# Kernel optimization log

Hardware: AMD Instinct MI355X
Metric: run time of the kernel (lower is better)

The kernel has to match this reference:

```python
import jax, jax.numpy as jnp
import numpy as np
from jax import lax

VOCAB = 32000; D = 1024; NL = 4; DI = 2048; S = 16; R = 64; DC = 4
B = 1; L = 1024; EPS = 1e-5


def setup_inputs() -> dict:
    key = jax.random.key(0)
    ks = jax.random.split(key, 16)
    def n(k, shape, s=0.02):
        return jax.random.normal(k, shape, dtype=jnp.float32) * s
    return dict(
        tokens=jax.random.randint(ks[0], (B, L), 0, VOCAB),
        embed=n(ks[1], (VOCAB, D)),
        norm_w=jnp.ones((NL, D), jnp.float32) + n(ks[2], (NL, D)),
        in_proj_w=n(ks[3], (NL, 2 * DI, D)),
        conv_w=n(ks[4], (NL, DI, DC), 0.1),
        conv_b=n(ks[5], (NL, DI)),
        x_proj_w=n(ks[6], (NL, R + 2 * S, DI)),
        dt_proj_w=n(ks[7], (NL, DI, R), 0.1),
        dt_proj_b=n(ks[8], (NL, DI), 0.5),
        A_log=n(ks[9], (NL, DI, S), 0.5),
        D_param=jnp.ones((NL, DI), jnp.float32) + n(ks[10], (NL, DI)),
        out_proj_w=n(ks[11], (NL, D, DI)),
        norm_f_w=jnp.ones((D,), jnp.float32),
        lm_head_w=n(ks[12], (VOCAB, D)),
    )


def _rmsnorm(x, w):
    return x * lax.rsqrt(jnp.mean(x * x, axis=-1, keepdims=True) + EPS) * w


def _mamba_block(x, norm_w, in_w, cw, cb, xw, dtw, dtb, a_log, dp, ow):
    # x: [B, L, D]
    res = x
    x = _rmsnorm(x, norm_w)
    xz = jnp.einsum('bld,ed->ble', x, in_w)      # [B, L, 2*DI]
    u, z = xz[..., :DI], xz[..., DI:]
    # depthwise causal conv over time
    u = jnp.swapaxes(u, 1, 2)                    # [B, DI, L]
    u = lax.conv_general_dilated(u, cw[:, None, :], (1,), [(DC - 1, 0)],
                                 feature_group_count=DI,
                                 dimension_numbers=('NCH', 'OIH', 'NCH'))
    u = jax.nn.silu(u + cb[None, :, None])
    u = jnp.swapaxes(u, 1, 2)                    # [B, L, DI]
    # input-dependent SSM params
    dbc = jnp.einsum('bld,ed->ble', u, xw)       # [B, L, R+2S]
    dt = jax.nn.softplus(jnp.einsum('blr,dr->bld', dbc[..., :R], dtw) + dtb)
    Bm = dbc[..., R:R + S]                       # [B, L, S]
    Cm = dbc[..., R + S:]                        # [B, L, S]
    A = -jnp.exp(a_log)                          # [DI, S]
    dA = jnp.exp(dt[..., None] * A)              # [B, L, DI, S]
    dBu = (dt * u)[..., None] * Bm[:, :, None, :]  # [B, L, DI, S]
    # selective scan over time
    def step(h, inp):
        a_t, b_t, c_t = inp
        h = a_t * h + b_t                        # [B, DI, S]
        y = jnp.einsum('bds,bs->bd', h, c_t)
        return h, y
    h0 = jnp.zeros((x.shape[0], DI, S), x.dtype)
    _, ys = lax.scan(step, h0, (jnp.moveaxis(dA, 1, 0), jnp.moveaxis(dBu, 1, 0), jnp.moveaxis(Cm, 1, 0)))
    y = jnp.moveaxis(ys, 0, 1) + u * dp          # [B, L, DI]
    y = y * jax.nn.silu(z)
    return res + jnp.einsum('bld,od->blo', y, ow)


def reference(tokens, embed, norm_w, in_proj_w, conv_w, conv_b, x_proj_w,
              dt_proj_w, dt_proj_b, A_log, D_param, out_proj_w, norm_f_w, lm_head_w):
    x = embed[tokens]                            # [B, L, D]
    for i in range(NL):
        x = _mamba_block(x, norm_w[i], in_proj_w[i], conv_w[i], conv_b[i],
                         x_proj_w[i], dt_proj_w[i], dt_proj_b[i], A_log[i],
                         D_param[i], out_proj_w[i])
    x = _rmsnorm(x, norm_f_w)
    return jnp.einsum('bld,vd->blv', x, lm_head_w)  # [B, L, VOCAB]
```

## Files before the change

kernel.cpp:

```cpp
#include <hip/hip_runtime.h>
#include <hip/hip_bf16.h>
#include <math.h>


typedef __attribute__((ext_vector_type(8))) short bf16x8;
typedef __attribute__((ext_vector_type(4))) float f32x4;

__device__ __forceinline__ short f2bf(float f) {
  union { float f; unsigned u; } v; v.f = f;
  unsigned u = v.u;
  unsigned r = (u + 0x7FFFu + ((u >> 16) & 1u)) >> 16;
  return (short)r;
}

__device__ __forceinline__ bf16x8 pack8(float4 a, float4 b) {
  bf16x8 r;
  r[0] = f2bf(a.x); r[1] = f2bf(a.y); r[2] = f2bf(a.z); r[3] = f2bf(a.w);
  r[4] = f2bf(b.x); r[5] = f2bf(b.y); r[6] = f2bf(b.z); r[7] = f2bf(b.w);
  return r;
}

__device__ __forceinline__ unsigned cvtpk(float lo, float hi) {
  unsigned r;
  asm("v_cvt_pk_bf16_f32 %0, %1, %2" : "=v"(r) : "v"(lo), "v"(hi));
  return r;
}

__device__ __forceinline__ float softplus_f(float x) {
  return (x > 20.f) ? x : log1pf(__expf(x));
}

__device__ __forceinline__ void gl_lds16(const void* g, void* l) {
  void* gnc = (void*)g;
  __builtin_amdgcn_global_load_lds((__attribute__((address_space(1))) void*)gnc,
                                   (__attribute__((address_space(3))) void*)l, 16, 0, 0);
}

__global__ __launch_bounds__(256) void cvt4_k(const float* __restrict__ s0, unsigned short* __restrict__ d0, int nb0,
                                              const float* __restrict__ s1, unsigned short* __restrict__ d1, int nb1,
                                              const float* __restrict__ s2, unsigned short* __restrict__ d2, int nb2,
                                              const float* __restrict__ s3, unsigned short* __restrict__ d3, int nb3) {
  int b = blockIdx.x;
  const float* s; unsigned short* d; int lb;
  if (b < nb0) { s = s0; d = d0; lb = b; }
  else if (b < nb0 + nb1) { s = s1; d = d1; lb = b - nb0; }
  else if (b < nb0 + nb1 + nb2) { s = s2; d = d2; lb = b - nb0 - nb1; }
  else { s = s3; d = d3; lb = b - nb0 - nb1 - nb2; }
  size_t base = (size_t)lb * 1024;
#pragma unroll
  for (int u = 0; u < 4; ++u) {
    size_t idx = base + u * 256 + threadIdx.x;
    const float4* p = (const float4*)(s + idx * 8);
    float4 a = p[0], bq = p[1];
    uint4 w;
    w.x = cvtpk(a.x, a.y); w.y = cvtpk(a.z, a.w);
    w.z = cvtpk(bq.x, bq.y); w.w = cvtpk(bq.z, bq.w);
    *(uint4*)(d + idx * 8) = w;
  }
}

__global__ __launch_bounds__(256) void embed_rms_k(const int* __restrict__ tok,
                                                   const float* __restrict__ emb,
                                                   const float* __restrict__ w,
                                                   float* __restrict__ x,
                                                   unsigned short* __restrict__ xn16) {
  int l = blockIdx.x;
  int t = tok[l];
  float4 v = ((const float4*)(emb + (size_t)t * 1024))[threadIdx.x];
  ((float4*)(x + (size_t)l * 1024))[threadIdx.x] = v;
  float ss = v.x * v.x + v.y * v.y + v.z * v.z + v.w * v.w;
  ss += __shfl_down(ss, 32); ss += __shfl_down(ss, 16); ss += __shfl_down(ss, 8);
  ss += __shfl_down(ss, 4);  ss += __shfl_down(ss, 2);  ss += __shfl_down(ss, 1);
  __shared__ float wsum[4];
  if ((threadIdx.x & 63) == 0) wsum[threadIdx.x >> 6] = ss;
  __syncthreads();
  float tot = wsum[0] + wsum[1] + wsum[2] + wsum[3];
  float sc = rsqrtf(tot * (1.0f / 1024.0f) + 1e-5f);
  float4 wv = ((const float4*)w)[threadIdx.x];
  ushort4 o;
  o.x = (unsigned short)f2bf(v.x * sc * wv.x);
  o.y = (unsigned short)f2bf(v.y * sc * wv.y);
  o.z = (unsigned short)f2bf(v.z * sc * wv.z);
  o.w = (unsigned short)f2bf(v.w * sc * wv.w);
  *(ushort4*)(xn16 + (size_t)l * 1024 + threadIdx.x * 4) = o;
}

__global__ __launch_bounds__(256) void rmsnorm16_k(const float* __restrict__ x,
                                                   const float* __restrict__ w,
                                                   unsigned short* __restrict__ y) {
  int l = blockIdx.x;
  const float4* xr = (const float4*)(x + (size_t)l * 1024);
  float4 v = xr[threadIdx.x];
  float ss = v.x * v.x + v.y * v.y + v.z * v.z + v.w * v.w;
  ss += __shfl_down(ss, 32); ss += __shfl_down(ss, 16); ss += __shfl_down(ss, 8);
  ss += __shfl_down(ss, 4);  ss += __shfl_down(ss, 2);  ss += __shfl_down(ss, 1);
  __shared__ float wsum[4];
  if ((threadIdx.x & 63) == 0) wsum[threadIdx.x >> 6] = ss;
  __syncthreads();
  float tot = wsum[0] + wsum[1] + wsum[2] + wsum[3];
  float sc = rsqrtf(tot * (1.0f / 1024.0f) + 1e-5f);
  float4 wv = ((const float4*)w)[threadIdx.x];
  ushort4 o;
  o.x = (unsigned short)f2bf(v.x * sc * wv.x);
  o.y = (unsigned short)f2bf(v.y * sc * wv.y);
  o.z = (unsigned short)f2bf(v.z * sc * wv.z);
  o.w = (unsigned short)f2bf(v.w * sc * wv.w);
  *(ushort4*)(y + (size_t)l * 1024 + threadIdx.x * 4) = o;
}

__global__ __launch_bounds__(256) void rmsnorm_k(const float* __restrict__ x,
                                                 const float* __restrict__ w,
                                                 float* __restrict__ y) {
  int l = blockIdx.x;
  const float4* xr = (const float4*)(x + (size_t)l * 1024);
  float4 v = xr[threadIdx.x];
  float ss = v.x * v.x + v.y * v.y + v.z * v.z + v.w * v.w;
  ss += __shfl_down(ss, 32); ss += __shfl_down(ss, 16); ss += __shfl_down(ss, 8);
  ss += __shfl_down(ss, 4);  ss += __shfl_down(ss, 2);  ss += __shfl_down(ss, 1);
  __shared__ float wsum[4];
  if ((threadIdx.x & 63) == 0) wsum[threadIdx.x >> 6] = ss;
  __syncthreads();
  float tot = wsum[0] + wsum[1] + wsum[2] + wsum[3];
  float sc = rsqrtf(tot * (1.0f / 1024.0f) + 1e-5f);
  float4 wv = ((const float4*)w)[threadIdx.x];
  float4 o;
  o.x = v.x * sc * wv.x; o.y = v.y * sc * wv.y;
  o.z = v.z * sc * wv.z; o.w = v.w * sc * wv.w;
  ((float4*)(y + (size_t)l * 1024))[threadIdx.x] = o;
}

__global__ __launch_bounds__(256) void conv_silu_k(const float* __restrict__ xz,
                                                   const float* __restrict__ cw,
                                                   const float* __restrict__ cb,
                                                   float* __restrict__ u,
                                                   unsigned short* __restrict__ u16) {
  int idx = blockIdx.x * 256 + threadIdx.x;
  int d = idx & 2047;
  int l = idx >> 11;
  float acc = cb[d];
#pragma unroll
  for (int j = 0; j < 4; ++j) {
    int ll = l - 3 + j;
    if (ll >= 0) acc = fmaf(xz[(size_t)ll * 4096 + d], cw[d * 4 + j], acc);
  }
  float sig = 1.0f / (1.0f + __expf(-acc));
  float v = acc * sig;
  u[idx] = v;
  if (u16) u16[idx] = (unsigned short)f2bf(v);
}

__global__ __launch_bounds__(256) void gemm16_k(const unsigned short* __restrict__ A, int lda,
                                                const unsigned short* __restrict__ W, int ldw,
                                                const float* __restrict__ addsrc,
                                                const float* __restrict__ spbias,
                                                float* __restrict__ C, int ldc,
                                                unsigned short* __restrict__ C16,
                                                int gx, int N, int K) {
  int total = gridDim.x;
  int lin = blockIdx.x;
  int q = total >> 3, r = total & 7;
  int xcd = lin & 7, idx = lin >> 3;
  int nl = (xcd < r ? xcd * (q + 1) : r * (q + 1) + (xcd - r) * q) + idx;
  const int bm = (nl % gx) << 7;
  const int bn = (nl / gx) << 7;

  const int tid = threadIdx.x;
  const int wid = tid >> 6;
  const int lane = tid & 63;
  const int wm = (wid >> 1) << 6;
  const int wn = (wid & 1) << 6;
  const int fr = lane & 15;
  const int kg = lane >> 4;
  const int srow = lane >> 3;
  const int sch  = lane & 7;
  const int xch  = sch ^ srow;

  __shared__ unsigned short sA[2][8192];
  __shared__ unsigned short sB[2][8192];

  f32x4 acc[4][4];
#pragma unroll
  for (int i = 0; i < 4; ++i)
#pragma unroll
    for (int j = 0; j < 4; ++j) acc[i][j] = (f32x4){0.f, 0.f, 0.f, 0.f};

  auto STAGE = [&](int b, int k0) {
#pragma unroll
    for (int t = 0; t < 4; ++t) {
      int g = (wid << 2) + t;
      int row = (g << 3) + srow;
      const unsigned short* ga = A + (size_t)(bm + row) * lda + k0 + (xch << 3);
      int wrow = bn + row; if (wrow >= N) wrow = N - 1;
      const unsigned short* gw = W + (size_t)wrow * ldw + k0 + (xch << 3);
      gl_lds16(ga, &sA[b][g << 9]);
      gl_lds16(gw, &sB[b][g << 9]);
    }
  };

  auto COMPUTE = [&](int b) {
#pragma unroll
    for (int ks = 0; ks < 2; ++ks) {
      bf16x8 af[4], bw[4];
#pragma unroll
      for (int mi = 0; mi < 4; ++mi) {
        int row = wm + (mi << 4) + fr;
        int xc = ((ks << 2) + kg) ^ (fr & 7);
        af[mi] = *(const bf16x8*)&sA[b][(row << 6) + (xc << 3)];
      }
#pragma unroll
      for (int ni = 0; ni < 4; ++ni) {
        int row = wn + (ni << 4) + fr;
        int xc = ((ks << 2) + kg) ^ (fr & 7);
        bw[ni] = *(const bf16x8*)&sB[b][(row << 6) + (xc << 3)];
      }
#pragma unroll
      for (int mi = 0; mi < 4; ++mi)
#pragma unroll
        for (int ni = 0; ni < 4; ++ni)
          acc[mi][ni] = __builtin_amdgcn_mfma_f32_16x16x32_bf16(af[mi], bw[ni], acc[mi][ni], 0, 0, 0);
    }
  };

  const int nt = K >> 6;
  STAGE(0, 0);
  int cur = 0;
  for (int t = 0; t + 1 < nt; ++t) {
    STAGE(cur ^ 1, (t + 1) << 6);
    asm volatile("s_waitcnt vmcnt(8)" ::: "memory");
    __builtin_amdgcn_s_barrier();
    __builtin_amdgcn_sched_barrier(0);
    COMPUTE(cur);
    __builtin_amdgcn_s_barrier();
    cur ^= 1;
  }
  asm volatile("s_waitcnt vmcnt(0)" ::: "memory");
  __builtin_amdgcn_s_barrier();
  __builtin_amdgcn_sched_barrier(0);
  COMPUTE(cur);

#pragma unroll
  for (int mi = 0; mi < 4; ++mi)
#pragma unroll
    for (int ni = 0; ni < 4; ++ni) {
      int n = bn + wn + (ni << 4) + fr;
      if (n < N) {
#pragma unroll
        for (int i = 0; i < 4; ++i) {
          int m = bm + wm + (mi << 4) + (kg << 2) + i;
          size_t off = (size_t)m * ldc + n;
          float v = acc[mi][ni][i];
          if (addsrc) v += addsrc[off];
          if (spbias) v = softplus_f(v + spbias[n]);
          C[off] = v;
          if (C16) C16[off] = (unsigned short)f2bf(v);
        }
      }
    }
}

__global__ __launch_bounds__(256) void gemm16sk_k(const unsigned short* __restrict__ A, int lda,
                                                  const unsigned short* __restrict__ W, int ldw,
                                                  float* __restrict__ Cp, int ldc,
                                                  int gx, int N, int Kchunk, int Mtot) {
  int total = gridDim.x;
  int lin = blockIdx.x;
  int q = total >> 3, r = total & 7;
  int xcd = lin & 7, idx = lin >> 3;
  int nl = (xcd < r ? xcd * (q + 1) : r * (q + 1) + (xcd - r) * q) + idx;
  const int bm = (nl % gx) << 7;
  const int bn = (nl / gx) << 7;
  const int ksplit = blockIdx.y;
  const int kbase = ksplit * Kchunk;

  const int tid = threadIdx.x;
  const int wid = tid >> 6;
  const int lane = tid & 63;
  const int wm = (wid >> 1) << 6;
  const int wn = (wid & 1) << 6;
  const int fr = lane & 15;
  const int kg = lane >> 4;
  const int srow = lane >> 3;
  const int sch  = lane & 7;
  const int xch  = sch ^ srow;

  __shared__ unsigned short sA[2][8192];
  __shared__ unsigned short sB[2][8192];

  f32x4 acc[4][4];
#pragma unroll
  for (int i = 0; i < 4; ++i)
#pragma unroll
    for (int j = 0; j < 4; ++j) acc[i][j] = (f32x4){0.f, 0.f, 0.f, 0.f};

  auto STAGE = [&](int b, int k0) {
#pragma unroll
    for (int t = 0; t < 4; ++t) {
      int g = (wid << 2) + t;
      int row = (g << 3) + srow;
      const unsigned short* ga = A + (size_t)(bm + row) * lda + k0 + (xch << 3);
      int wrow = bn + row; if (wrow >= N) wrow = N - 1;
      const unsigned short* gw = W + (size_t)wrow * ldw + k0 + (xch << 3);
      gl_lds16(ga, &sA[b][g << 9]);
      gl_lds16(gw, &sB[b][g << 9]);
    }
  };

  auto COMPUTE = [&](int b) {
#pragma unroll
    for (int ks = 0; ks < 2; ++ks) {
      bf16x8 af[4], bw[4];
#pragma unroll
      for (int mi = 0; mi < 4; ++mi) {
        int row = wm + (mi << 4) + fr;
        int xc = ((ks << 2) + kg) ^ (fr & 7);
        af[mi] = *(const bf16x8*)&sA[b][(row << 6) + (xc << 3)];
      }
#pragma unroll
      for (int ni = 0; ni < 4; ++ni) {
        int row = wn + (ni << 4) + fr;
        int xc = ((ks << 2) + kg) ^ (fr & 7);
        bw[ni] = *(const bf16x8*)&sB[b][(row << 6) + (xc << 3)];
      }
#pragma unroll
      for (int mi = 0; mi < 4; ++mi)
#pragma unroll
        for (int ni = 0; ni < 4; ++ni)
          acc[mi][ni] = __builtin_amdgcn_mfma_f32_16x16x32_bf16(af[mi], bw[ni], acc[mi][ni], 0, 0, 0);
    }
  };

  const int nt = Kchunk >> 6;
  STAGE(0, kbase);
  int cur = 0;
  for (int t = 0; t + 1 < nt; ++t) {
    STAGE(cur ^ 1, kbase + ((t + 1) << 6));
    asm volatile("s_waitcnt vmcnt(8)" ::: "memory");
    __builtin_amdgcn_s_barrier();
    __builtin_amdgcn_sched_barrier(0);
    COMPUTE(cur);
    __builtin_amdgcn_s_barrier();
    cur ^= 1;
  }
  asm volatile("s_waitcnt vmcnt(0)" ::: "memory");
  __builtin_amdgcn_s_barrier();
  __builtin_amdgcn_sched_barrier(0);
  COMPUTE(cur);

  float* Cs = Cp + (size_t)ksplit * Mtot * ldc;
#pragma unroll
  for (int mi = 0; mi < 4; ++mi)
#pragma unroll
    for (int ni = 0; ni < 4; ++ni) {
      int n = bn + wn + (ni << 4) + fr;
      if (n < N) {
#pragma unroll
        for (int i = 0; i < 4; ++i) {
          int m = bm + wm + (mi << 4) + (kg << 2) + i;
          Cs[(size_t)m * ldc + n] = acc[mi][ni][i];
        }
      }
    }
}

__global__ __launch_bounds__(256) void reduce_xp_k(const float* __restrict__ Cp,
                                                   float* __restrict__ dbc,
                                                   unsigned short* __restrict__ dbc16) {
  int i = blockIdx.x * 256 + threadIdx.x;
  float v = Cp[i] + Cp[98304 + i] + Cp[2 * 98304 + i] + Cp[3 * 98304 + i];
  dbc[i] = v;
  dbc16[i] = (unsigned short)f2bf(v);
}

__global__ __launch_bounds__(256) void reduce_op_k(const float* __restrict__ Cp,
                                                   float* __restrict__ x) {
  int i = blockIdx.x * 256 + threadIdx.x;
  const float4* p0 = (const float4*)Cp;
  const float4* p1 = (const float4*)(Cp + 1048576);
  const float4* p2 = (const float4*)(Cp + 2097152);
  const float4* p3 = (const float4*)(Cp + 3145728);
  float4 a = p0[i], b = p1[i], c = p2[i], d = p3[i];
  float4 xv = ((float4*)x)[i];
  xv.x += a.x + b.x + c.x + d.x;
  xv.y += a.y + b.y + c.y + d.y;
  xv.z += a.z + b.z + c.z + d.z;
  xv.w += a.w + b.w + c.w + d.w;
  ((float4*)x)[i] = xv;
}

struct WREG { float4 v[8]; };

__global__ __launch_bounds__(512) void gemm256f_k(const unsigned short* __restrict__ A, int lda,
                                                  const float* __restrict__ W, int ldw,
                                                  float* __restrict__ C, int ldc,
                                                  int gx, int N, int K) {
  int total = gridDim.x;
  int lin = blockIdx.x;
  int q = total >> 3, r = total & 7;
  int xcd = lin & 7, idx = lin >> 3;
  int nl = (xcd < r ? xcd * (q + 1) : r * (q + 1) + (xcd - r) * q) + idx;
  const int bm = (nl % gx) << 8;
  const int bn = (nl / gx) << 8;

  const int tid = threadIdx.x;
  const int wid = tid >> 6;
  const int lane = tid & 63;
  const int wm = (wid >> 2) << 7;
  const int wn = (wid & 3) << 6;
  const int fr = lane & 15;
  const int kg = lane >> 4;
  const int srow = lane >> 3;
  const int sch  = lane & 7;
  const int xch  = sch ^ srow;

  const int wr_row  = tid >> 1;
  const int wr_half = tid & 1;
  int wr_grow = bn + wr_row; if (wr_grow >= N) wr_grow = N - 1;
  const float* gWrow = W + (size_t)wr_grow * ldw + wr_half * 32;

  __shared__ unsigned short sA[2][16384];
  __shared__ unsigned short sB[2][16384];

  f32x4 acc[8][4];
#pragma unroll
  for (int i = 0; i < 8; ++i)
#pragma unroll
    for (int j = 0; j < 4; ++j) acc[i][j] = (f32x4){0.f, 0.f, 0.f, 0.f};

  auto STAGE_A = [&](unsigned short* buf, int k0) {
#pragma unroll
    for (int t = 0; t < 4; ++t) {
      int g = (wid << 2) + t;
      int row = (g << 3) + srow;
      const unsigned short* ga = A + (size_t)(bm + row) * lda + k0 + (xch << 3);
      gl_lds16(ga, &buf[g << 9]);
    }
  };

  auto WLOAD = [&](WREG& w, int k0) {
    const float4* p = (const float4*)(gWrow + k0);
#pragma unroll
    for (int j = 0; j < 8; ++j) w.v[j] = p[j];
  };

  auto WWRITE = [&](unsigned short* buf, const WREG& w) {
#pragma unroll
    for (int c2 = 0; c2 < 4; ++c2) {
      int c = (wr_half << 2) + c2;
      uint4 val;
      val.x = cvtpk(w.v[2 * c2].x,     w.v[2 * c2].y);
      val.y = cvtpk(w.v[2 * c2].z,     w.v[2 * c2].w);
      val.z = cvtpk(w.v[2 * c2 + 1].x, w.v[2 * c2 + 1].y);
      val.w = cvtpk(w.v[2 * c2 + 1].z, w.v[2 * c2 + 1].w);
      *(uint4*)&buf[(wr_row << 6) + ((c ^ (wr_row & 7)) << 3)] = val;
    }
  };

  auto COMPUTE = [&](const unsigned short* bufa, const unsigned short* bufb) {
#pragma unroll
    for (int ks = 0; ks < 2; ++ks) {
      bf16x8 af[8], bw[4];
#pragma unroll
      for (int mi = 0; mi < 8; ++mi) {
        int row = wm + (mi << 4) + fr;
        int xc = ((ks << 2) + kg) ^ (fr & 7);
        af[mi] = *(const bf16x8*)&bufa[(row << 6) + (xc << 3)];
      }
#pragma unroll
      for (int ni = 0; ni < 4; ++ni) {
        int row = wn + (ni << 4) + fr;
        int xc = ((ks << 2) + kg) ^ (fr & 7);
        bw[ni] = *(const bf16x8*)&bufb[(row << 6) + (xc << 3)];
      }
#pragma unroll
      for (int mi = 0; mi < 8; ++mi)
#pragma unroll
        for (int ni = 0; ni < 4; ++ni)
          acc[mi][ni] = __builtin_amdgcn_mfma_f32_16x16x32_bf16(af[mi], bw[ni], acc[mi][ni], 0, 0, 0);
    }
  };

  const int nt = K >> 6;
  WREG wrA, wrB;

  STAGE_A(sA[0], 0);
  WLOAD(wrA, 0);
  STAGE_A(sA[1], 64);
  WLOAD(wrB, 64);
  __builtin_amdgcn_sched_barrier(0);
  asm volatile("s_waitcnt vmcnt(12)" ::: "memory");
  __builtin_amdgcn_sched_barrier(0);
  WWRITE(sB[0], wrA);
  asm volatile("s_waitcnt lgkmcnt(0)" ::: "memory");
  __builtin_amdgcn_s_barrier();
  __builtin_amdgcn_sched_barrier(0);

  for (int tt = 0; tt < nt; tt += 2) {
    COMPUTE(sA[0], sB[0]);
    __builtin_amdgcn_s_barrier();
    if (tt + 2 < nt) {
      STAGE_A(sA[0], (tt + 2) << 6);
      WLOAD(wrA, (tt + 2) << 6);
      __builtin_amdgcn_sched_barrier(0);
      asm volatile("s_waitcnt vmcnt(12)" ::: "memory");
    } else {
      asm volatile("s_waitcnt vmcnt(0)" ::: "memory");
    }
    __builtin_amdgcn_sched_barrier(0);
    WWRITE(sB[1], wrB);
    asm volatile("s_waitcnt lgkmcnt(0)" ::: "memory");
    __builtin_amdgcn_s_barrier();
    __builtin_amdgcn_sched_barrier(0);

    COMPUTE(sA[1], sB[1]);
    if (tt + 2 < nt) {
      __builtin_amdgcn_s_barrier();
      if (tt + 3 < nt) {
        STAGE_A(sA[1], (tt + 3) << 6);
        WLOAD(wrB, (tt + 3) << 6);
        __builtin_amdgcn_sched_barrier(0);
        asm volatile("s_waitcnt vmcnt(12)" ::: "memory");
      } else {
        asm volatile("s_waitcnt vmcnt(0)" ::: "memory");
      }
      __builtin_amdgcn_sched_barrier(0);
      WWRITE(sB[0], wrA);
      asm volatile("s_waitcnt lgkmcnt(0)" ::: "memory");
      __builtin_amdgcn_s_barrier();
      __builtin_amdgcn_sched_barrier(0);
    }
  }

#pragma unroll
  for (int mi = 0; mi < 8; ++mi)
#pragma unroll
    for (int ni = 0; ni < 4; ++ni) {
      int n = bn + wn + (ni << 4) + fr;
      if (n < N) {
#pragma unroll
        for (int i = 0; i < 4; ++i) {
          int m = bm + wm + (mi << 4) + (kg << 2) + i;
          C[(size_t)m * ldc + n] = acc[mi][ni][i];
        }
      }
    }
}

__global__ __launch_bounds__(256) void gemm_bt_k(const float* __restrict__ A, int lda,
                                                 const float* __restrict__ W, int ldw,
                                                 const float* __restrict__ addsrc,
                                                 float* __restrict__ C, int ldc,
                                                 int N, int K) {
  const int tid  = threadIdx.x;
  const int srow = tid >> 1;
  const int skg  = (tid & 1) << 1;
  const int bm = blockIdx.x << 7;
  const int bn = blockIdx.y << 7;
  const int wid = tid >> 6;
  const int lane = tid & 63;
  const int wm = (wid >> 1) << 6;
  const int wn = (wid & 1) << 6;
  const int fr = lane & 15;
  const int kg = lane >> 4;

  __shared__ bf16x8 lA[4][128];
  __shared__ bf16x8 lB[4][128];

  f32x4 zero4 = {0.f, 0.f, 0.f, 0.f};
  f32x4 acc[4][4];
#pragma unroll
  for (int i = 0; i < 4; ++i)
#pragma unroll
    for (int j = 0; j < 4; ++j) acc[i][j] = zero4;

  const bool wvalid = (bn + srow) < N;
  const float* gA = A + (size_t)(bm + srow) * lda + (skg << 3);
  const float* gW = W + (size_t)(wvalid ? (bn + srow) : 0) * ldw + (skg << 3);

  for (int k0 = 0; k0 < K; k0 += 32) {
    float4 a0 = *(const float4*)(gA + k0);
    float4 a1 = *(const float4*)(gA + k0 + 4);
    float4 a2 = *(const float4*)(gA + k0 + 8);
    float4 a3 = *(const float4*)(gA + k0 + 12);
    float4 w0 = make_float4(0.f, 0.f, 0.f, 0.f), w1 = w0, w2 = w0, w3 = w0;
    if (wvalid) {
      w0 = *(const float4*)(gW + k0);
      w1 = *(const float4*)(gW + k0 + 4);
      w2 = *(const float4*)(gW + k0 + 8);
      w3 = *(const float4*)(gW + k0 + 12);
    }
    __syncthreads();
    lA[skg][srow]     = pack8(a0, a1);
    lA[skg + 1][srow] = pack8(a2, a3);
    lB[skg][srow]     = pack8(w0, w1);
    lB[skg + 1][srow] = pack8(w2, w3);
    __syncthreads();

    bf16x8 af[4], bf_[4];
#pragma unroll
    for (int mi = 0; mi < 4; ++mi) af[mi] = lA[kg][wm + (mi << 4) + fr];
#pragma unroll
    for (int ni = 0; ni < 4; ++ni) bf_[ni] = lB[kg][wn + (ni << 4) + fr];
#pragma unroll
    for (int mi = 0; mi < 4; ++mi)
#pragma unroll
      for (int ni = 0; ni < 4; ++ni)
        acc[mi][ni] = __builtin_amdgcn_mfma_f32_16x16x32_bf16(af[mi], bf_[ni], acc[mi][ni], 0, 0, 0);
  }

#pragma unroll
  for (int mi = 0; mi < 4; ++mi)
#pragma unroll
    for (int ni = 0; ni < 4; ++ni) {
      int n = bn + wn + (ni << 4) + fr;
      if (n < N) {
#pragma unroll
        for (int i = 0; i < 4; ++i) {
          int m = bm + wm + (mi << 4) + (kg << 2) + i;
          size_t off = (size_t)m * ldc + n;
          float v = acc[mi][ni][i];
          if (addsrc) v += addsrc[off];
          C[off] = v;
        }
      }
    }
}

#define NCH 32
#define CHL 32

__global__ __launch_bounds__(256) void scan_p1f_k(const float* __restrict__ dtv,
                                                  const float* __restrict__ u,
                                                  const float* __restrict__ dbc,
                                                  const float* __restrict__ A_log,
                                                  float* __restrict__ Pg,
                                                  float* __restrict__ qg) {
  int tid = threadIdx.x;
  int s = tid & 15, dg = tid >> 4;
  int d = (blockIdx.x << 4) + dg;
  int c = blockIdx.y;
  int l0 = c << 5;
  float A = -__expf(A_log[d * 16 + s]);
  float P = 1.f, q = 0.f;
#pragma unroll 4
  for (int i = 0; i < CHL; ++i) {
    int l = l0 + i;
    size_t rd = (size_t)l * 2048 + d;
    float dt = dtv[rd];
    float dA = __expf(dt * A);
    P *= dA;
    q = fmaf(dA, q, dt * u[rd] * dbc[l * 96 + 64 + s]);
  }
  size_t o = (size_t)c * 32768 + d * 16 + s;
  Pg[o] = P;
  qg[o] = q;
}

__global__ __launch_bounds__(256) void scan_p3f_k(const float* __restrict__ dtv,
                                                  const float* __restrict__ u,
                                                  const float* __restrict__ dbc,
                                                  const float* __restrict__ xz,
                                                  const float* __restrict__ A_log,
                                                  const float* __restrict__ Dp,
                                                  const float* __restrict__ Pg,
                                                  const float* __restrict__ qg,
                                                  unsigned short* __restrict__ y16) {
  int tid = threadIdx.x;
  int s = tid & 15, dg = tid >> 4;
  int d = (blockIdx.x << 4) + dg;
  int c = blockIdx.y;
  int l0 = c << 5;
  float A = -__expf(A_log[d * 16 + s]);
  float dpar = Dp[d];
  float h = 0.f;
  for (int cc = 0; cc < c; ++cc) {
    size_t o = (size_t)cc * 32768 + d * 16 + s;
    h = fmaf(Pg[o], h, qg[o]);
  }
#pragma unroll 4
  for (int i = 0; i < CHL; ++i) {
    int l = l0 + i;
    size_t rd = (size_t)l * 2048 + d;
    float dt = dtv[rd];
    float uv = u[rd];
    float dA = __expf(dt * A);
    h = fmaf(dA, h, dt * uv * dbc[l * 96 + 64 + s]);
    float p = h * dbc[l * 96 + 80 + s];
    p += __shfl_xor(p, 1); p += __shfl_xor(p, 2);
    p += __shfl_xor(p, 4); p += __shfl_xor(p, 8);
    if (s == 0) {
      float zv = xz[(size_t)l * 4096 + 2048 + d];
      float sig = 1.0f / (1.0f + __expf(-zv));
      y16[rd] = (unsigned short)f2bf((p + uv * dpar) * (zv * sig));
    }
  }
}

__global__ __launch_bounds__(256) void scan_p1_k(const float* __restrict__ dtr,
                                                 const float* __restrict__ u,
                                                 const float* __restrict__ dbc,
                                                 const float* __restrict__ A_log,
                                                 const float* __restrict__ dtb,
                                                 float* __restrict__ Pg,
                                                 float* __restrict__ qg) {
  int tid = threadIdx.x;
  int s = tid & 15, dg = tid >> 4;
  int d = (blockIdx.x << 4) + dg;
  int c = blockIdx.y;
  int l0 = c << 5;
  float A = -__expf(A_log[d * 16 + s]);
  float bias = dtb[d];
  float P = 1.f, q = 0.f;
#pragma unroll 4
  for (int i = 0; i < CHL; ++i) {
    int l = l0 + i;
    float dt = softplus_f(dtr[(size_t)l * 2048 + d] + bias);
    float dA = __expf(dt * A);
    P *= dA;
    q = fmaf(dA, q, dt * u[(size_t)l * 2048 + d] * dbc[l * 96 + 64 + s]);
  }
  size_t o = (size_t)c * 32768 + d * 16 + s;
  Pg[o] = P;
  qg[o] = q;
}

__global__ __launch_bounds__(256) void scan_p2_k(const float* __restrict__ Pg,
                                                 const float* __restrict__ qg,
                                                 float* __restrict__ hst) {
  int idx = blockIdx.x * 256 + threadIdx.x;
  float h = 0.f;
#pragma unroll
  for (int c = 0; c < NCH; ++c) {
    size_t o = (size_t)c * 32768 + idx;
    hst[o] = h;
    h = fmaf(Pg[o], h, qg[o]);
  }
}

__global__ __launch_bounds__(256) void scan_p3_k(const float* __restrict__ dtr,
                                                 const float* __restrict__ u,
                                                 const float* __restrict__ dbc,
                                                 const float* __restrict__ xz,
                                                 const float* __restrict__ A_log,
                                                 const float* __restrict__ Dp,
                                                 const float* __restrict__ dtb,
                                                 const float* __restrict__ hst,
                                                 float* __restrict__ y) {
  int tid = threadIdx.x;
  int s = tid & 15, dg = tid >> 4;
  int d = (blockIdx.x << 4) + dg;
  int c = blockIdx.y;
  int l0 = c << 5;
  float A = -__expf(A_log[d * 16 + s]);
  float dpar = Dp[d];
  float bias = dtb[d];
  float h = hst[(size_t)c * 32768 + d * 16 + s];
#pragma unroll 4
  for (int i = 0; i < CHL; ++i) {
    int l = l0 + i;
    size_t rd = (size_t)l * 2048 + d;
    float dt = softplus_f(dtr[rd] + bias);
    float uv = u[rd];
    float dA = __expf(dt * A);
    h = fmaf(dA, h, dt * uv * dbc[l * 96 + 64 + s]);
    float p = h * dbc[l * 96 + 80 + s];
    p += __shfl_xor(p, 1); p += __shfl_xor(p, 2);
    p += __shfl_xor(p, 4); p += __shfl_xor(p, 8);
    if (s == 0) {
      float zv = xz[(size_t)l * 4096 + 2048 + d];
      float sig = 1.0f / (1.0f + __expf(-zv));
      y[rd] = (p + uv * dpar) * (zv * sig);
    }
  }
}

extern "C" void kernel_launch(void* const* d_in, const int* in_sizes, int n_in,
                              void* d_out, int out_size, void* d_ws, size_t ws_size,
                              hipStream_t stream) {
  const int*   tokens = (const int*)d_in[0];
  const float* embed  = (const float*)d_in[1];
  const float* norm_w = (const float*)d_in[2];
  const float* in_w   = (const float*)d_in[3];
  const float* conv_w = (const float*)d_in[4];
  const float* conv_b = (const float*)d_in[5];
  const float* x_w    = (const float*)d_in[6];
  const float* dt_w   = (const float*)d_in[7];
  const float* dt_b   = (const float*)d_in[8];
  const float* A_log  = (const float*)d_in[9];
  const float* D_par  = (const float*)d_in[10];
  const float* out_w  = (const float*)d_in[11];
  const float* normf  = (const float*)d_in[12];
  const float* lm_w   = (const float*)d_in[13];

  float* out = (float*)d_out;
  float* x    = out;
  float* xz   = x    + 1024 * 1024;
  float* u    = xz   + 1024 * 4096;
  float* dtv  = u    + 1024 * 2048;
  float* dbc  = dtv  + 1024 * 2048;
  float* Pg   = dbc  + 1024 * 96;
  float* qg   = Pg   + 32 * 32768;
  float* hst  = qg   + 32 * 32768;
  float* xn_f = hst  + 32 * 32768;
  float* y_f  = xn_f + 1024 * 1024;
  unsigned short* xn16  = (unsigned short*)(y_f + 1024 * 2048);
  unsigned short* u16   = xn16 + 1024 * 1024;
  unsigned short* y16   = u16  + 1024 * 2048;
  unsigned short* dbc16 = y16  + 1024 * 2048;
  float* part_op = (float*)(dbc16 + 1024 * 96);
  float* part_xp = part_op + 4 * 1048576;

  unsigned short* inw16 = (unsigned short*)d_ws;
  unsigned short* oww16 = inw16 + 16777216;
  unsigned short* xw16  = oww16 + 8388608;
  unsigned short* dtw16 = xw16  + 786432;
  unsigned short* xnf16 = dtw16 + 524288;
  const size_t need = (size_t)(16777216 + 8388608 + 786432 + 524288 + 1048576) * 2;
  const bool fast = ws_size >= need;

  if (fast) {
    cvt4_k<<<3232, 256, 0, stream>>>(in_w, inw16, 2048,
                                     out_w, oww16, 1024,
                                     x_w, xw16, 96,
                                     dt_w, dtw16, 64);
    embed_rms_k<<<1024, 256, 0, stream>>>(tokens, embed, norm_w, x, xn16);

    for (int i = 0; i < 4; ++i) {
      if (i > 0) rmsnorm16_k<<<1024, 256, 0, stream>>>(x, norm_w + i * 1024, xn16);
      gemm16_k<<<256, 256, 0, stream>>>(xn16, 1024, inw16 + (size_t)i * 4194304, 1024,
                                        nullptr, nullptr, xz, 4096, nullptr, 8, 4096, 1024);
      conv_silu_k<<<8192, 256, 0, stream>>>(xz, conv_w + i * 8192, conv_b + i * 2048, u, u16);
      gemm16sk_k<<<dim3(8, 4), 256, 0, stream>>>(u16, 2048, xw16 + (size_t)i * 196608, 2048,
                                                 part_xp, 96, 8, 96, 512, 1024);
      reduce_xp_k<<<384, 256, 0, stream>>>(part_xp, dbc, dbc16);
      gemm16_k<<<128, 256, 0, stream>>>(dbc16, 96, dtw16 + (size_t)i * 131072, 64,
                                        nullptr, dt_b + i * 2048, dtv, 2048, nullptr, 8, 2048, 64);
      scan_p1f_k<<<dim3(128, NCH), 256, 0, stream>>>(dtv, u, dbc, A_log + i * 32768, Pg, qg);
      scan_p3f_k<<<dim3(128, NCH), 256, 0, stream>>>(dtv, u, dbc, xz, A_log + i * 32768,
                                                     D_par + i * 2048, Pg, qg, y16);
      gemm16sk_k<<<dim3(64, 4), 256, 0, stream>>>(y16, 2048, oww16 + (size_t)i * 2097152, 2048,
                                                  part_op, 1024, 8, 1024, 512, 1024);
      reduce_op_k<<<1024, 256, 0, stream>>>(part_op, x);
    }

    rmsnorm16_k<<<1024, 256, 0, stream>>>(x, normf, xnf16);
    gemm256f_k<<<500, 512, 0, stream>>>(xnf16, 1024, lm_w, 1024, out, 32000, 4, 32000, 1024);
  } else {
    float* xnf_f = (float*)d_ws;
    embed_rms_k<<<1024, 256, 0, stream>>>(tokens, embed, norm_w, x, xn16);
    for (int i = 0; i < 4; ++i) {
      rmsnorm_k<<<1024, 256, 0, stream>>>(x, norm_w + i * 1024, xn_f);
      gemm_bt_k<<<dim3(8, 32), 256, 0, stream>>>(xn_f, 1024, in_w + (size_t)i * 4194304, 1024,
                                                 nullptr, xz, 4096, 4096, 1024);
      conv_silu_k<<<8192, 256, 0, stream>>>(xz, conv_w + i * 8192, conv_b + i * 2048, u, nullptr);
      gemm_bt_k<<<dim3(8, 1), 256, 0, stream>>>(u, 2048, x_w + (size_t)i * 196608, 2048,
                                                nullptr, dbc, 96, 96, 2048);
      gemm_bt_k<<<dim3(8, 16), 256, 0, stream>>>(dbc, 96, dt_w + (size_t)i * 131072, 64,
                                                 nullptr, dtv, 2048, 2048, 64);
      scan_p1_k<<<dim3(128, NCH), 256, 0, stream>>>(dtv, u, dbc, A_log + i * 32768,
                                                    dt_b + i * 2048, Pg, qg);
      scan_p2_k<<<128, 256, 0, stream>>>(Pg, qg, hst);
      scan_p3_k<<<dim3(128, NCH), 256, 0, stream>>>(dtv, u, dbc, xz, A_log + i * 32768,
                                                    D_par + i * 2048, dt_b + i * 2048, hst, y_f);
      gemm_bt_k<<<dim3(8, 8), 256, 0, stream>>>(y_f, 2048, out_w + (size_t)i * 2097152, 2048,
                                                x, x, 1024, 1024, 2048);
    }
    rmsnorm_k<<<1024, 256, 0, stream>>>(x, normf, xnf_f);
    gemm_bt_k<<<dim3(8, 250), 256, 0, stream>>>(xnf_f, 1024, lm_w, 1024,
                                                nullptr, out, 32000, 32000, 1024);
  }
}
```

Before: 1.037 ms.

## Single-register-set weight prefetch pipeline with two-block occupancy hint in gemm256f

Restructures the 256x256 GEMM main loop, which converts fp32 weights to bf16 on the fly. It goes from a two-deep register prefetch (two weight register sets, loads issued two tiles ahead) to a one-deep prefetch using a single register set, with loads for tile t+1 issued before computing tile t. The launch bounds are raised to request 2 blocks per CU, which caps registers per thread. The intent is to improve occupancy and latency hiding. The cost is less prefetch distance: a full vmcnt(0) wait now happens every iteration, and a tighter register budget could cause spills with 128 accumulator registers.

```diff
diff --git a/kernel.cpp b/kernel.cpp
--- a/kernel.cpp
+++ b/kernel.cpp
@@ -389,10 +389,10 @@
 
 struct WREG { float4 v[8]; };
 
-__global__ __launch_bounds__(512) void gemm256f_k(const unsigned short* __restrict__ A, int lda,
-                                                  const float* __restrict__ W, int ldw,
-                                                  float* __restrict__ C, int ldc,
-                                                  int gx, int N, int K) {
+__global__ __launch_bounds__(512, 2) void gemm256f_k(const unsigned short* __restrict__ A, int lda,
+                                                     const float* __restrict__ W, int ldw,
+                                                     float* __restrict__ C, int ldc,
+                                                     int gx, int N, int K) {
   int total = gridDim.x;
   int lin = blockIdx.x;
   int q = total >> 3, r = total & 7;
@@ -436,21 +436,22 @@
     }
   };
 
-  auto WLOAD = [&](WREG& w, int k0) {
+  WREG wr;
+  auto WLOAD = [&](int k0) {
     const float4* p = (const float4*)(gWrow + k0);
 #pragma unroll
-    for (int j = 0; j < 8; ++j) w.v[j] = p[j];
+    for (int j = 0; j < 8; ++j) wr.v[j] = p[j];
   };
 
-  auto WWRITE = [&](unsigned short* buf, const WREG& w) {
+  auto WWRITE = [&](unsigned short* buf) {
 #pragma unroll
     for (int c2 = 0; c2 < 4; ++c2) {
       int c = (wr_half << 2) + c2;
       uint4 val;
-      val.x = cvtpk(w.v[2 * c2].x,     w.v[2 * c2].y);
-      val.y = cvtpk(w.v[2 * c2].z,     w.v[2 * c2].w);
-      val.z = cvtpk(w.v[2 * c2 + 1].x, w.v[2 * c2 + 1].y);
-      val.w = cvtpk(w.v[2 * c2 + 1].z, w.v[2 * c2 + 1].w);
+      val.x = cvtpk(wr.v[2 * c2].x,     wr.v[2 * c2].y);
+      val.y = cvtpk(wr.v[2 * c2].z,     wr.v[2 * c2].w);
+      val.z = cvtpk(wr.v[2 * c2 + 1].x, wr.v[2 * c2 + 1].y);
+      val.w = cvtpk(wr.v[2 * c2 + 1].z, wr.v[2 * c2 + 1].w);
       *(uint4*)&buf[(wr_row << 6) + ((c ^ (wr_row & 7)) << 3)] = val;
     }
   };
@@ -480,53 +481,33 @@
   };
 
   const int nt = K >> 6;
-  WREG wrA, wrB;
 
   STAGE_A(sA[0], 0);
-  WLOAD(wrA, 0);
-  STAGE_A(sA[1], 64);
-  WLOAD(wrB, 64);
+  WLOAD(0);
+  asm volatile("s_waitcnt vmcnt(0)" ::: "memory");
   __builtin_amdgcn_sched_barrier(0);
-  asm volatile("s_waitcnt vmcnt(12)" ::: "memory");
-  __builtin_amdgcn_sched_barrier(0);
-  WWRITE(sB[0], wrA);
+  WWRITE(sB[0]);
   asm volatile("s_waitcnt lgkmcnt(0)" ::: "memory");
   __builtin_amdgcn_s_barrier();
   __builtin_amdgcn_sched_barrier(0);
 
-  for (int tt = 0; tt < nt; tt += 2) {
-    COMPUTE(sA[0], sB[0]);
+  int cur = 0;
+  for (int t = 0; t < nt; ++t) {
+    if (t + 1 < nt) {
+      STAGE_A(sA[cur ^ 1], (t + 1) << 6);
+      WLOAD((t + 1) << 6);
+      __builtin_amdgcn_sched_barrier(0);
+    }
+    COMPUTE(sA[cur], sB[cur]);
     __builtin_amdgcn_s_barrier();
-    if (tt + 2 < nt) {
-      STAGE_A(sA[0], (tt + 2) << 6);
-      WLOAD(wrA, (tt + 2) << 6);
+    if (t + 1 < nt) {
+      asm volatile("s_waitcnt vmcnt(0)" ::: "memory");
       __builtin_amdgcn_sched_barrier(0);
-      asm volatile("s_waitcnt vmcnt(12)" ::: "memory");
-    } else {
-      asm volatile("s_waitcnt vmcnt(0)" ::: "memory");
-    }
-    __builtin_amdgcn_sched_barrier(0);
-    WWRITE(sB[1], wrB);
-    asm volatile("s_waitcnt lgkmcnt(0)" ::: "memory");
-    __builtin_amdgcn_s_barrier();
-    __builtin_amdgcn_sched_barrier(0);
-
-    COMPUTE(sA[1], sB[1]);
-    if (tt + 2 < nt) {
-      __builtin_amdgcn_s_barrier();
-      if (tt + 3 < nt) {
-        STAGE_A(sA[1], (tt + 3) << 6);
-        WLOAD(wrB, (tt + 3) << 6);
-        __builtin_amdgcn_sched_barrier(0);
-        asm volatile("s_waitcnt vmcnt(12)" ::: "memory");
-      } else {
-        asm volatile("s_waitcnt vmcnt(0)" ::: "memory");
-      }
-      __builtin_amdgcn_sched_barrier(0);
-      WWRITE(sB[0], wrA);
+      WWRITE(sB[cur ^ 1]);
       asm volatile("s_waitcnt lgkmcnt(0)" ::: "memory");
       __builtin_amdgcn_s_barrier();
       __builtin_amdgcn_sched_barrier(0);
+      cur ^= 1;
     }
   }
 
```

Result: faster. 943.8 us (-9.0%).
